# Optimization experiments

Measured on AMD Instinct MI355X. Metric: run time of the kernel, lower is better.

## Reference

```python
import jax, jax.numpy as jnp
import numpy as np

B, S, D, H, NL, FE = 2, 1024, 1024, 16, 6, 4
HD = D // H
DFF = D * FE
EPS = 1e-5


def setup_inputs() -> dict:
    key = jax.random.key(0)
    ks = jax.random.split(key, 12)
    sd = 0.02
    n = lambda k, sh: (jax.random.normal(k, sh, jnp.float32) * sd)
    return {
        "x": jax.random.normal(ks[0], (B, S, D), jnp.float32),
        "pos": n(ks[1], (1, S, D)),
        "Wq": n(ks[2], (NL, HD, HD)), "bq": jnp.zeros((NL, HD), jnp.float32),
        "Wk": n(ks[3], (NL, HD, HD)), "bk": jnp.zeros((NL, HD), jnp.float32),
        "Wv": n(ks[4], (NL, HD, HD)), "bv": jnp.zeros((NL, HD), jnp.float32),
        "Wfc": n(ks[5], (NL, D, D)), "bfc": jnp.zeros((NL, D), jnp.float32),
        "ln1_w": jnp.ones((NL, D), jnp.float32), "ln1_b": jnp.zeros((NL, D), jnp.float32),
        "ln2_w": jnp.ones((NL, D), jnp.float32), "ln2_b": jnp.zeros((NL, D), jnp.float32),
        "W1": n(ks[6], (NL, D, DFF)), "b1": jnp.zeros((NL, DFF), jnp.float32),
        "W2": n(ks[7], (NL, DFF, D)), "b2": jnp.zeros((NL, D), jnp.float32),
        "lnf_w": jnp.ones((D,), jnp.float32), "lnf_b": jnp.zeros((D,), jnp.float32),
    }


def _ln(z, w, b):
    m = jnp.mean(z, axis=-1, keepdims=True)
    v = jnp.mean(jnp.square(z - m), axis=-1, keepdims=True)
    return (z - m) * jax.lax.rsqrt(v + EPS) * w + b


def reference(x, pos, Wq, bq, Wk, bk, Wv, bv, Wfc, bfc,
              ln1_w, ln1_b, ln2_w, ln2_b, W1, b1, W2, b2, lnf_w, lnf_b):
    Bx, Sx, Dx = x.shape
    causal = jnp.tril(jnp.ones((Sx, Sx), bool))  # [S,S], broadcast over b,h
    y = x + pos[:, :Sx, :]
    scale = 1.0 / jnp.sqrt(jnp.float32(HD))
    for i in range(NL):
        yh = y.reshape(Bx, Sx, H, HD)
        # per-head Linear with weights SHARED across heads (as in source)
        q = yh @ Wq[i] + bq[i]
        k = yh @ Wk[i] + bk[i]
        v = yh @ Wv[i] + bv[i]
        score = jnp.einsum("bqhd,bkhd->bhqk", q, k)
        # masked_fill(-1e20) BEFORE scaling, as in source
        score = jnp.where(causal, score, jnp.float32(-1e20)) * scale
        attn = jax.nn.softmax(score, axis=-1)
        o = jnp.einsum("bhqk,bkhd->bqhd", attn, v).reshape(Bx, Sx, D)
        o = o @ Wfc[i] + bfc[i]
        add = _ln(o + y, ln1_w[i], ln1_b[i])
        ff = jax.nn.gelu(add @ W1[i] + b1[i], approximate=False) @ W2[i] + b2[i]
        y = _ln(ff + add, ln2_w[i], ln2_b[i])
    return _ln(y, lnf_w, lnf_b)
```

## Files before the change

### kernel.cpp

```cpp
#include <hip/hip_runtime.h>
#include <hip/hip_bf16.h>
#include <math.h>

#define B_   2
#define S_   1024
#define D_   1024
#define H_   16
#define HD_  64
#define NL_  6
#define DFF_ 4096

typedef __bf16 bf16_t;
typedef bf16_t bf16x8 __attribute__((ext_vector_type(8)));
typedef bf16_t bf16x4 __attribute__((ext_vector_type(4)));
typedef float  f32x4  __attribute__((ext_vector_type(4)));

__device__ __forceinline__ float gelu_exact(float x) {
    return 0.5f * x * (1.0f + erff(x * 0.70710678118654752f));
}

__global__ __launch_bounds__(256) void add_pos_kernel(
    const float* __restrict__ x, const float* __restrict__ pos,
    float* __restrict__ y, bf16_t* __restrict__ yb)
{
    int idx = blockIdx.x * 256 + threadIdx.x;
    f32x4 xv = *(const f32x4*)&x[idx * 4];
    f32x4 pv = *(const f32x4*)&pos[(idx & 262143) * 4];
    f32x4 o = xv + pv;
    *(f32x4*)&y[idx * 4] = o;
    *(bf16x4*)&yb[idx * 4] = __builtin_convertvector(o, bf16x4);
}

__global__ __launch_bounds__(256) void qkv_mfma_kernel(
    const bf16_t* __restrict__ yb,
    const float* __restrict__ Wq, const float* __restrict__ bq,
    const float* __restrict__ Wk, const float* __restrict__ bk,
    const float* __restrict__ Wv, const float* __restrict__ bv,
    bf16_t* __restrict__ q, bf16_t* __restrict__ k, bf16_t* __restrict__ v)
{
    __shared__ bf16_t As[128][72];
    __shared__ bf16_t Wt[3][64][72];

    int tid = threadIdx.x;
    long m0 = (long)blockIdx.x * 128;

#pragma unroll
    for (int it = 0; it < 4; ++it) {
        int c = it * 256 + tid;
        int row = c >> 3, col = (c & 7) * 8;
        *(bf16x8*)&As[row][col] = *(const bf16x8*)&yb[(m0 + row) * 64 + col];
    }
#pragma unroll
    for (int it = 0; it < 16; ++it) {
        int i = it * 256 + tid;
        int r = i >> 6, c = i & 63;
        Wt[0][c][r] = (bf16_t)Wq[i];
        Wt[1][c][r] = (bf16_t)Wk[i];
        Wt[2][c][r] = (bf16_t)Wv[i];
    }
    __syncthreads();

    int wave = tid >> 6, lane = tid & 63;
    int quad = lane >> 4, l16 = lane & 15;
    int wm = wave * 32;

    bf16x8 a[2][2];
#pragma unroll
    for (int i = 0; i < 2; ++i)
#pragma unroll
        for (int ks = 0; ks < 2; ++ks)
            a[i][ks] = *(bf16x8*)&As[wm + i * 16 + l16][ks * 32 + quad * 8];

    f32x4 acc[3][2][4];
#pragma unroll
    for (int o = 0; o < 3; ++o)
#pragma unroll
        for (int i = 0; i < 2; ++i)
#pragma unroll
            for (int j = 0; j < 4; ++j) acc[o][i][j] = (f32x4)0.f;

#pragma unroll
    for (int o = 0; o < 3; ++o)
#pragma unroll
        for (int j = 0; j < 4; ++j) {
            bf16x8 b0 = *(bf16x8*)&Wt[o][j * 16 + l16][quad * 8];
            bf16x8 b1 = *(bf16x8*)&Wt[o][j * 16 + l16][32 + quad * 8];
#pragma unroll
            for (int i = 0; i < 2; ++i) {
                acc[o][i][j] = __builtin_amdgcn_mfma_f32_16x16x32_bf16(a[i][0], b0, acc[o][i][j], 0, 0, 0);
                acc[o][i][j] = __builtin_amdgcn_mfma_f32_16x16x32_bf16(a[i][1], b1, acc[o][i][j], 0, 0, 0);
            }
        }

    bf16_t* outs[3] = { q, k, v };
    const float* biases[3] = { bq, bk, bv };
#pragma unroll
    for (int o = 0; o < 3; ++o)
#pragma unroll
        for (int j = 0; j < 4; ++j) {
            int col = j * 16 + l16;
            float bias = biases[o][col];
#pragma unroll
            for (int i = 0; i < 2; ++i) {
                long rbase = m0 + wm + i * 16 + quad * 4;
#pragma unroll
                for (int r = 0; r < 4; ++r)
                    outs[o][(rbase + r) * 64 + col] = (bf16_t)(acc[o][i][j][r] + bias);
            }
        }
}

__global__ __launch_bounds__(256) void vtrans_kernel(
    const bf16_t* __restrict__ vb, bf16_t* __restrict__ vT)
{
    __shared__ bf16_t L[32][72];
    int tid = threadIdx.x;
    int s0 = blockIdx.x * 32;
    int bh = blockIdx.y;
    int b = bh >> 4, h = bh & 15;
    int sr = tid >> 3, dc = (tid & 7) * 8;
    *(bf16x8*)&L[sr][dc] =
        *(const bf16x8*)&vb[(((long)b * S_ + s0 + sr) * H_ + h) * HD_ + dc];
    __syncthreads();
    int dr = tid >> 2, sg = (tid & 3) * 8;
    bf16x8 o;
#pragma unroll
    for (int j = 0; j < 8; ++j) o[j] = L[sg + j][dr];
    *(bf16x8*)&vT[((long)bh * HD_ + dr) * S_ + s0 + sg] = o;
}

__global__ __launch_bounds__(256) void attn_mfma_kernel(
    const bf16_t* __restrict__ Q, const bf16_t* __restrict__ K,
    const bf16_t* __restrict__ VT, bf16_t* __restrict__ Ob)
{
    __shared__ bf16_t Ks[32][72];
    __shared__ bf16_t Vt[64][40];
    __shared__ bf16_t Ps[4][16][40];

    int tid = threadIdx.x;
    int wave = tid >> 6, lane = tid & 63;
    int quad = lane >> 4, l16 = lane & 15;
    int q0 = blockIdx.x * 64;
    int bh = blockIdx.y;
    int b = bh >> 4, h = bh & 15;
    int qw = q0 + wave * 16;
    const float scale = 0.125f;
    const float MASKED = -1.25e19f;

    const bf16_t* Qbase = Q + (((long)b * S_ + qw + l16) * H_ + h) * HD_;
    bf16x8 aq0 = *(const bf16x8*)&Qbase[quad * 8];
    bf16x8 aq1 = *(const bf16x8*)&Qbase[32 + quad * 8];

    float mrun = -3.0e38f, lrun = 0.f;
    f32x4 oacc[4];
#pragma unroll
    for (int n = 0; n < 4; ++n) oacc[n] = (f32x4)0.f;

    int srow = tid >> 3, scol = (tid & 7) * 8;
    int vdr = tid >> 2, vkg = (tid & 3) * 8;
    const bf16_t* VTbase = VT + ((long)bh * HD_ + vdr) * S_ + vkg;
    int qg = qw + l16;

    int nkt = (q0 + 64) / 32;
    for (int kt = 0; kt < nkt; ++kt) {
        int k0 = kt * 32;
        __syncthreads();
        *(bf16x8*)&Ks[srow][scol] =
            *(const bf16x8*)&K[(((long)b * S_ + k0 + srow) * H_ + h) * HD_ + scol];
        *(bf16x8*)&Vt[vdr][vkg] = *(const bf16x8*)&VTbase[k0];
        __syncthreads();

        if (k0 > qw + 15) continue;

        f32x4 sc[2];
        sc[0] = (f32x4)0.f; sc[1] = (f32x4)0.f;
#pragma unroll
        for (int n = 0; n < 2; ++n) {
            bf16x8 ak0 = *(bf16x8*)&Ks[n * 16 + l16][quad * 8];
            bf16x8 ak1 = *(bf16x8*)&Ks[n * 16 + l16][32 + quad * 8];
            sc[n] = __builtin_amdgcn_mfma_f32_16x16x32_bf16(ak0, aq0, sc[n], 0, 0, 0);
            sc[n] = __builtin_amdgcn_mfma_f32_16x16x32_bf16(ak1, aq1, sc[n], 0, 0, 0);
        }
        float pmax = MASKED;
#pragma unroll
        for (int n = 0; n < 2; ++n)
#pragma unroll
            for (int r = 0; r < 4; ++r) {
                int kv = k0 + n * 16 + quad * 4 + r;
                float sv = (kv <= qg) ? sc[n][r] * scale : MASKED;
                sc[n][r] = sv;
                pmax = fmaxf(pmax, sv);
            }
        pmax = fmaxf(pmax, __shfl_xor(pmax, 16));
        pmax = fmaxf(pmax, __shfl_xor(pmax, 32));
        float mnew = fmaxf(mrun, pmax);
        float ls = 0.f;
#pragma unroll
        for (int n = 0; n < 2; ++n)
#pragma unroll
            for (int r = 0; r < 4; ++r) {
                float pv = __expf(sc[n][r] - mnew);
                sc[n][r] = pv;
                ls += pv;
            }
        ls += __shfl_xor(ls, 16);
        ls += __shfl_xor(ls, 32);
        float alpha = __expf(mrun - mnew);
        lrun = lrun * alpha + ls;
        mrun = mnew;

        *(bf16x4*)&Ps[wave][l16][quad * 4]      = __builtin_convertvector(sc[0], bf16x4);
        *(bf16x4*)&Ps[wave][l16][16 + quad * 4] = __builtin_convertvector(sc[1], bf16x4);

        f32x4 av;
#pragma unroll
        for (int r = 0; r < 4; ++r) av[r] = __shfl(alpha, quad * 4 + r);

        bf16x8 pa = *(bf16x8*)&Ps[wave][l16][quad * 8];
#pragma unroll
        for (int n = 0; n < 4; ++n) {
            bf16x8 bv = *(bf16x8*)&Vt[n * 16 + l16][quad * 8];
            oacc[n] = __builtin_amdgcn_mfma_f32_16x16x32_bf16(pa, bv, oacc[n] * av, 0, 0, 0);
        }
    }

    float inv = 1.0f / lrun;
    f32x4 iv;
#pragma unroll
    for (int r = 0; r < 4; ++r) iv[r] = __shfl(inv, quad * 4 + r);
#pragma unroll
    for (int r = 0; r < 4; ++r) {
        long rowbase = (((long)b * S_ + qw + quad * 4 + r) * H_ + h) * HD_;
#pragma unroll
        for (int n = 0; n < 4; ++n)
            Ob[rowbase + n * 16 + l16] = (bf16_t)(oacc[n][r] * iv[r]);
    }
}

__global__ void tconv_kernel(const float* __restrict__ W, bf16_t* __restrict__ Wt,
                             int Kd, int Nd)
{
    __shared__ float t[32][33];
    int tx = threadIdx.x, ty = threadIdx.y;
    int bx = blockIdx.x, by = blockIdx.y;
#pragma unroll
    for (int i = 0; i < 4; ++i)
        t[ty + i * 8][tx] = W[(size_t)(by * 32 + ty + i * 8) * Nd + bx * 32 + tx];
    __syncthreads();
#pragma unroll
    for (int i = 0; i < 4; ++i)
        Wt[(size_t)(bx * 32 + ty + i * 8) * Kd + by * 32 + tx] = (bf16_t)t[tx][ty + i * 8];
}

#define LDT 40
template<int BN>
__global__ __launch_bounds__(256) void gemm_bt_kernel(
    const bf16_t* __restrict__ A, const bf16_t* __restrict__ Bt,
    const float* __restrict__ bias, float* __restrict__ Cf,
    bf16_t* __restrict__ Cb, int M, int N, int K, int act, size_t pstride)
{
    __shared__ bf16_t As[128 * LDT];
    __shared__ bf16_t Bs[BN * LDT];
    int tid = threadIdx.x;
    int wave = tid >> 6, lane = tid & 63;
    int quad = lane >> 4, l16 = lane & 15;
    int m0 = blockIdx.x * 128;
    int n0 = blockIdx.y * BN;
    int Kc = K / gridDim.z;
    int kbeg = blockIdx.z * Kc;
    int kend = kbeg + Kc;
    float* Cfp = Cf ? Cf + (size_t)blockIdx.z * pstride : nullptr;

    constexpr int WN = BN / 2;
    constexpr int NJ = WN / 16;
    int wm = (wave >> 1) * 64, wn = (wave & 1) * WN;

    f32x4 acc[4][NJ];
#pragma unroll
    for (int i = 0; i < 4; ++i)
#pragma unroll
        for (int j = 0; j < NJ; ++j) acc[i][j] = (f32x4)0.f;

    for (int k0 = kbeg; k0 < kend; k0 += 32) {
        __syncthreads();
#pragma unroll
        for (int it = 0; it < 2; ++it) {
            int c = it * 256 + tid;
            int row = c >> 2, col = (c & 3) * 8;
            *(bf16x8*)&As[row * LDT + col] =
                *(const bf16x8*)&A[(size_t)(m0 + row) * K + k0 + col];
        }
#pragma unroll
        for (int it = 0; it < BN / 64; ++it) {
            int c = it * 256 + tid;
            int row = c >> 2, col = (c & 3) * 8;
            *(bf16x8*)&Bs[row * LDT + col] =
                *(const bf16x8*)&Bt[(size_t)(n0 + row) * K + k0 + col];
        }
        __syncthreads();

        bf16x8 af[4], bfr[NJ];
#pragma unroll
        for (int i = 0; i < 4; ++i)
            af[i] = *(bf16x8*)&As[(wm + i * 16 + l16) * LDT + quad * 8];
#pragma unroll
        for (int j = 0; j < NJ; ++j)
            bfr[j] = *(bf16x8*)&Bs[(wn + j * 16 + l16) * LDT + quad * 8];
#pragma unroll
        for (int i = 0; i < 4; ++i)
#pragma unroll
            for (int j = 0; j < NJ; ++j)
                acc[i][j] = __builtin_amdgcn_mfma_f32_16x16x32_bf16(
                    af[i], bfr[j], acc[i][j], 0, 0, 0);
    }

#pragma unroll
    for (int j = 0; j < NJ; ++j) {
        int col = n0 + wn + j * 16 + l16;
        float bv = (bias && blockIdx.z == 0) ? bias[col] : 0.f;
#pragma unroll
        for (int i = 0; i < 4; ++i) {
            int rbase = m0 + wm + i * 16 + quad * 4;
#pragma unroll
            for (int r = 0; r < 4; ++r) {
                float vv = acc[i][j][r] + bv;
                if (act == 1) vv = gelu_exact(vv);
                if (Cfp) Cfp[(size_t)(rbase + r) * N + col] = vv;
                if (Cb) Cb[(size_t)(rbase + r) * N + col] = (bf16_t)vv;
            }
        }
    }
}

__global__ __launch_bounds__(256) void ln_fused_kernel(
    const float* __restrict__ a0, const float* __restrict__ a1,
    const float* __restrict__ b,
    const float* __restrict__ w, const float* __restrict__ beta,
    float* __restrict__ out, bf16_t* __restrict__ outb)
{
    long row = blockIdx.x;
    int tid = threadIdx.x;
    f32x4 z = *(const f32x4*)&a0[row * D_ + tid * 4];
    if (a1) z += *(const f32x4*)&a1[row * D_ + tid * 4];
    if (b)  z += *(const f32x4*)&b[row * D_ + tid * 4];
    float s  = z[0] + z[1] + z[2] + z[3];
    float ss = z[0]*z[0] + z[1]*z[1] + z[2]*z[2] + z[3]*z[3];
#pragma unroll
    for (int off = 32; off >= 1; off >>= 1) {
        s  += __shfl_down(s, off);
        ss += __shfl_down(ss, off);
    }
    __shared__ float red[8];
    int lane = tid & 63, wid = tid >> 6;
    if (lane == 0) { red[wid * 2] = s; red[wid * 2 + 1] = ss; }
    __syncthreads();
    s  = red[0] + red[2] + red[4] + red[6];
    ss = red[1] + red[3] + red[5] + red[7];
    float mean = s * (1.0f / D_);
    float var  = ss * (1.0f / D_) - mean * mean;
    float rs = rsqrtf(var + 1e-5f);
    f32x4 wv = *(const f32x4*)&w[tid * 4];
    f32x4 bv = *(const f32x4*)&beta[tid * 4];
    f32x4 o = (z - mean) * rs * wv + bv;
    *(f32x4*)&out[row * D_ + tid * 4] = o;
    if (outb) *(bf16x4*)&outb[row * D_ + tid * 4] = __builtin_convertvector(o, bf16x4);
}

extern "C" void kernel_launch(void* const* d_in, const int* in_sizes, int n_in,
                              void* d_out, int out_size, void* d_ws, size_t ws_size,
                              hipStream_t stream)
{
    (void)in_sizes; (void)n_in; (void)out_size; (void)ws_size;
    const float* x    = (const float*)d_in[0];
    const float* pos  = (const float*)d_in[1];
    const float* Wq   = (const float*)d_in[2];
    const float* bq   = (const float*)d_in[3];
    const float* Wk   = (const float*)d_in[4];
    const float* bk   = (const float*)d_in[5];
    const float* Wv   = (const float*)d_in[6];
    const float* bv   = (const float*)d_in[7];
    const float* Wfc  = (const float*)d_in[8];
    const float* bfc  = (const float*)d_in[9];
    const float* ln1w = (const float*)d_in[10];
    const float* ln1b = (const float*)d_in[11];
    const float* ln2w = (const float*)d_in[12];
    const float* ln2b = (const float*)d_in[13];
    const float* W1   = (const float*)d_in[14];
    const float* b1   = (const float*)d_in[15];
    const float* W2   = (const float*)d_in[16];
    const float* b2   = (const float*)d_in[17];
    const float* lnfw = (const float*)d_in[18];
    const float* lnfb = (const float*)d_in[19];

    const size_t MB = 1 << 20;
    char* ws = (char*)d_ws;
    float*  y    = (float*)(ws);
    bf16_t* yb   = (bf16_t*)(ws + 8 * MB);
    bf16_t* qb   = (bf16_t*)(ws + 12 * MB);
    bf16_t* kb   = (bf16_t*)(ws + 16 * MB);
    bf16_t* vb   = (bf16_t*)(ws + 20 * MB);
    bf16_t* ob   = (bf16_t*)(ws + 24 * MB);
    float*  t1a  = (float*)(ws + 12 * MB);
    float*  t1b  = (float*)(ws + 28 * MB);
    float*  t2a  = (float*)(ws + 12 * MB);
    float*  t2b  = (float*)(ws + 20 * MB);
    float*  add  = (float*)(ws + 28 * MB);
    bf16_t* addb = (bf16_t*)(ws + 36 * MB);
    bf16_t* vTb  = (bf16_t*)(ws + 40 * MB);
    bf16_t* ffb  = (bf16_t*)(ws + 40 * MB);
    bf16_t* WT   = (bf16_t*)(ws + 56 * MB);

    const size_t pstride_wfc  = (size_t)16 * MB / sizeof(float);
    const size_t pstride_ffn2 = (size_t)8 * MB / sizeof(float);

    add_pos_kernel<<<2048, 256, 0, stream>>>(x, pos, y, yb);

    for (int i = 0; i < NL_; ++i) {
        qkv_mfma_kernel<<<256, 256, 0, stream>>>(
            yb, Wq + i * 4096, bq + i * 64, Wk + i * 4096, bk + i * 64,
            Wv + i * 4096, bv + i * 64, qb, kb, vb);

        vtrans_kernel<<<dim3(32, 32), 256, 0, stream>>>(vb, vTb);

        attn_mfma_kernel<<<dim3(16, 32), 256, 0, stream>>>(qb, kb, vTb, ob);

        tconv_kernel<<<dim3(32, 32), dim3(32, 8), 0, stream>>>(
            Wfc + (size_t)i * D_ * D_, WT, D_, D_);
        gemm_bt_kernel<64><<<dim3(16, 16, 2), 256, 0, stream>>>(
            ob, WT, bfc + i * D_, t1a, nullptr, 2048, D_, D_, 0, pstride_wfc);

        ln_fused_kernel<<<2048, 256, 0, stream>>>(
            t1a, t1b, y, ln1w + i * D_, ln1b + i * D_, add, addb);

        tconv_kernel<<<dim3(128, 32), dim3(32, 8), 0, stream>>>(
            W1 + (size_t)i * D_ * DFF_, WT, D_, DFF_);
        gemm_bt_kernel<128><<<dim3(16, 32, 1), 256, 0, stream>>>(
            addb, WT, b1 + i * DFF_, nullptr, ffb, 2048, DFF_, D_, 1, 0);

        tconv_kernel<<<dim3(32, 128), dim3(32, 8), 0, stream>>>(
            W2 + (size_t)i * DFF_ * D_, WT, DFF_, D_);
        gemm_bt_kernel<64><<<dim3(16, 16, 2), 256, 0, stream>>>(
            ffb, WT, b2 + i * D_, t2a, nullptr, 2048, D_, DFF_, 0, pstride_ffn2);

        ln_fused_kernel<<<2048, 256, 0, stream>>>(
            t2a, t2b, add, ln2w + i * D_, ln2b + i * D_, y, yb);
    }

    ln_fused_kernel<<<2048, 256, 0, stream>>>(
        y, nullptr, nullptr, lnfw, lnfb, (float*)d_out, nullptr);
}
```

Baseline: 1.354 ms.

## Load GEMM tiles directly into LDS with swizzled layout via global_load_lds

The GEMM kernel now stages A and B tiles with the direct global-to-LDS load builtin instead of loading through registers and storing to padded shared memory. An XOR swizzle on the 16-byte slots replaces the padding, so LDS reads avoid bank conflicts while the writes stay contiguous. The tile width is fixed at 64, and the FFN1 GEMM grid doubles to match, which gives more, smaller blocks there. Shared arrays elsewhere gain 16-byte alignment. The cost is less data reuse per block for FFN1 and a dependence on the exact wave-to-row mapping of the direct LDS load.

```diff
diff --git a/kernel.cpp b/kernel.cpp
--- a/kernel.cpp
+++ b/kernel.cpp
@@ -19,6 +19,12 @@
     return 0.5f * x * (1.0f + erff(x * 0.70710678118654752f));
 }
 
+__device__ __forceinline__ void gload16(const bf16_t* g, bf16_t* l) {
+    __builtin_amdgcn_global_load_lds(
+        (const __attribute__((address_space(1))) void*)g,
+        (__attribute__((address_space(3))) void*)l, 16, 0, 0);
+}
+
 __global__ __launch_bounds__(256) void add_pos_kernel(
     const float* __restrict__ x, const float* __restrict__ pos,
     float* __restrict__ y, bf16_t* __restrict__ yb)
@@ -38,8 +44,8 @@
     const float* __restrict__ Wv, const float* __restrict__ bv,
     bf16_t* __restrict__ q, bf16_t* __restrict__ k, bf16_t* __restrict__ v)
 {
-    __shared__ bf16_t As[128][72];
-    __shared__ bf16_t Wt[3][64][72];
+    __shared__ __align__(16) bf16_t As[128][72];
+    __shared__ __align__(16) bf16_t Wt[3][64][72];
 
     int tid = threadIdx.x;
     long m0 = (long)blockIdx.x * 128;
@@ -113,7 +119,7 @@
 __global__ __launch_bounds__(256) void vtrans_kernel(
     const bf16_t* __restrict__ vb, bf16_t* __restrict__ vT)
 {
-    __shared__ bf16_t L[32][72];
+    __shared__ __align__(16) bf16_t L[32][72];
     int tid = threadIdx.x;
     int s0 = blockIdx.x * 32;
     int bh = blockIdx.y;
@@ -133,9 +139,9 @@
     const bf16_t* __restrict__ Q, const bf16_t* __restrict__ K,
     const bf16_t* __restrict__ VT, bf16_t* __restrict__ Ob)
 {
-    __shared__ bf16_t Ks[32][72];
-    __shared__ bf16_t Vt[64][40];
-    __shared__ bf16_t Ps[4][16][40];
+    __shared__ __align__(16) bf16_t Ks[32][72];
+    __shared__ __align__(16) bf16_t Vt[64][40];
+    __shared__ __align__(16) bf16_t Ps[4][16][40];
 
     int tid = threadIdx.x;
     int wave = tid >> 6, lane = tid & 63;
@@ -252,70 +258,65 @@
         Wt[(size_t)(bx * 32 + ty + i * 8) * Kd + by * 32 + tx] = (bf16_t)t[tx][ty + i * 8];
 }
 
-#define LDT 40
-template<int BN>
 __global__ __launch_bounds__(256) void gemm_bt_kernel(
     const bf16_t* __restrict__ A, const bf16_t* __restrict__ Bt,
     const float* __restrict__ bias, float* __restrict__ Cf,
     bf16_t* __restrict__ Cb, int M, int N, int K, int act, size_t pstride)
 {
-    __shared__ bf16_t As[128 * LDT];
-    __shared__ bf16_t Bs[BN * LDT];
+    __shared__ __align__(16) bf16_t As[128 * 32];
+    __shared__ __align__(16) bf16_t Bs[64 * 32];
     int tid = threadIdx.x;
     int wave = tid >> 6, lane = tid & 63;
     int quad = lane >> 4, l16 = lane & 15;
     int m0 = blockIdx.x * 128;
-    int n0 = blockIdx.y * BN;
+    int n0 = blockIdx.y * 64;
     int Kc = K / gridDim.z;
     int kbeg = blockIdx.z * Kc;
     int kend = kbeg + Kc;
     float* Cfp = Cf ? Cf + (size_t)blockIdx.z * pstride : nullptr;
 
-    constexpr int WN = BN / 2;
-    constexpr int NJ = WN / 16;
-    int wm = (wave >> 1) * 64, wn = (wave & 1) * WN;
-
-    f32x4 acc[4][NJ];
+    int wm = (wave >> 1) * 64, wn = (wave & 1) * 32;
+
+    int srow = lane >> 2;
+    int sslot = (lane & 3) ^ (srow & 3);
+    int rslot = (quad ^ (l16 & 3)) * 8;
+
+    f32x4 acc[4][2];
 #pragma unroll
     for (int i = 0; i < 4; ++i)
 #pragma unroll
-        for (int j = 0; j < NJ; ++j) acc[i][j] = (f32x4)0.f;
+        for (int j = 0; j < 2; ++j) acc[i][j] = (f32x4)0.f;
+
+    const bf16_t* Ab = A + (size_t)(m0 + srow) * K + sslot * 8;
+    const bf16_t* Bb = Bt + (size_t)(n0 + wave * 16 + srow) * K + sslot * 8;
 
     for (int k0 = kbeg; k0 < kend; k0 += 32) {
         __syncthreads();
 #pragma unroll
-        for (int it = 0; it < 2; ++it) {
-            int c = it * 256 + tid;
-            int row = c >> 2, col = (c & 3) * 8;
-            *(bf16x8*)&As[row * LDT + col] =
-                *(const bf16x8*)&A[(size_t)(m0 + row) * K + k0 + col];
-        }
-#pragma unroll
-        for (int it = 0; it < BN / 64; ++it) {
-            int c = it * 256 + tid;
-            int row = c >> 2, col = (c & 3) * 8;
-            *(bf16x8*)&Bs[row * LDT + col] =
-                *(const bf16x8*)&Bt[(size_t)(n0 + row) * K + k0 + col];
-        }
+        for (int t = 0; t < 2; ++t) {
+            int seg = wave * 2 + t;
+            gload16(Ab + (size_t)seg * 16 * K + k0, &As[seg * 512]);
+        }
+        gload16(Bb + k0, &Bs[wave * 512]);
         __syncthreads();
 
-        bf16x8 af[4], bfr[NJ];
+        bf16x8 af[4], bfr[2];
 #pragma unroll
         for (int i = 0; i < 4; ++i)
-            af[i] = *(bf16x8*)&As[(wm + i * 16 + l16) * LDT + quad * 8];
-#pragma unroll
-        for (int j = 0; j < NJ; ++j)
-            bfr[j] = *(bf16x8*)&Bs[(wn + j * 16 + l16) * LDT + quad * 8];
+            af[i] = *(bf16x8*)&As[(wm + i * 16 + l16) * 32 + rslot];
+#pragma unroll
+        for (int j = 0; j < 2; ++j)
+            bfr[j] = *(bf16x8*)&Bs[(wn + j * 16 + l16) * 32 + rslot];
 #pragma unroll
         for (int i = 0; i < 4; ++i)
 #pragma unroll
-            for (int j = 0; j < NJ; ++j)
+            for (int j = 0; j < 2; ++j)
                 acc[i][j] = __builtin_amdgcn_mfma_f32_16x16x32_bf16(
                     af[i], bfr[j], acc[i][j], 0, 0, 0);
     }
 
 #pragma unroll
-    for (int j = 0; j < NJ; ++j) {
+    for (int j = 0; j < 2; ++j) {
         int col = n0 + wn + j * 16 + l16;
         float bv = (bias && blockIdx.z == 0) ? bias[col] : 0.f;
 #pragma unroll
@@ -426,7 +427,7 @@
 
         tconv_kernel<<<dim3(32, 32), dim3(32, 8), 0, stream>>>(
             Wfc + (size_t)i * D_ * D_, WT, D_, D_);
-        gemm_bt_kernel<64><<<dim3(16, 16, 2), 256, 0, stream>>>(
+        gemm_bt_kernel<<<dim3(16, 16, 2), 256, 0, stream>>>(
             ob, WT, bfc + i * D_, t1a, nullptr, 2048, D_, D_, 0, pstride_wfc);
 
         ln_fused_kernel<<<2048, 256, 0, stream>>>(
@@ -434,12 +435,12 @@
 
         tconv_kernel<<<dim3(128, 32), dim3(32, 8), 0, stream>>>(
             W1 + (size_t)i * D_ * DFF_, WT, D_, DFF_);
-        gemm_bt_kernel<128><<<dim3(16, 32, 1), 256, 0, stream>>>(
+        gemm_bt_kernel<<<dim3(16, 64, 1), 256, 0, stream>>>(
             addb, WT, b1 + i * DFF_, nullptr, ffb, 2048, DFF_, D_, 1, 0);
 
         tconv_kernel<<<dim3(32, 128), dim3(32, 8), 0, stream>>>(
             W2 + (size_t)i * DFF_ * D_, WT, DFF_, D_);
-        gemm_bt_kernel<64><<<dim3(16, 16, 2), 256, 0, stream>>>(
+        gemm_bt_kernel<<<dim3(16, 16, 2), 256, 0, stream>>>(
             ffb, WT, b2 + i * D_, t2a, nullptr, 2048, D_, DFF_, 0, pstride_ffn2);
 
         ln_fused_kernel<<<2048, 256, 0, stream>>>(
```

After: 1.294 ms. 4.4% less time.
